# Kernel tuning notes

Measured on AMD Instinct MI355X. Metric: run time of the kernel, lower is better.

## Reference

```python
import jax, jax.numpy as jnp
import numpy as np

N = 100000      # nodes
E = 3200000     # edges
IN, HID, OUT = 512, 256, 16
K = 10
ALPHA = 0.1


def setup_inputs() -> dict:
    key = jax.random.key(0)
    k1, k2, k3, k4 = jax.random.split(key, 4)
    x = jax.random.normal(k1, (N, IN), dtype=jnp.float32)
    edge_index = jax.random.randint(k2, (2, E), 0, N, dtype=jnp.int64)
    # torch.nn.Linear weights are [out_features, in_features]
    W1 = jax.random.normal(k3, (HID, IN), dtype=jnp.float32) * (1.0 / np.sqrt(IN))
    b1 = jnp.zeros((HID,), dtype=jnp.float32)
    W2 = jax.random.normal(k4, (OUT, HID), dtype=jnp.float32) * (1.0 / np.sqrt(HID))
    b2 = jnp.zeros((OUT,), dtype=jnp.float32)
    return {"x": x, "edge_index": edge_index, "W1": W1, "b1": b1, "W2": W2, "b2": b2}


def reference(x, edge_index, W1, b1, W2, b2):
    # Eval mode: dropout(p=0.5) is identity.
    h = jax.nn.relu(x @ W1.T + b1)           # [N, HID]
    h = h @ W2.T + b2                        # [N, OUT]

    # GCN normalization with self loops (PyG gcn_norm, add_self_loops=True)
    loop = jnp.arange(N, dtype=edge_index.dtype)
    row = jnp.concatenate([edge_index[0], loop])   # source (x_j)
    col = jnp.concatenate([edge_index[1], loop])   # target (aggregate here)
    deg = jax.ops.segment_sum(jnp.ones(row.shape[0], dtype=h.dtype), col, num_segments=N)
    dinv = jnp.where(deg > 0, deg ** -0.5, 0.0)
    norm = dinv[row] * dinv[col]                   # [E+N]

    # APPNP: z_{k+1} = (1-alpha) * A_hat z_k + alpha * h
    def step(z, _):
        msg = norm[:, None] * z[row]                                   # [E+N, OUT]
        agg = jax.ops.segment_sum(msg, col, num_segments=N)            # [N, OUT]
        return (1.0 - ALPHA) * agg + ALPHA * h, None

    z, _ = jax.lax.scan(step, h, None, length=K)
    return jax.nn.log_softmax(z, axis=1)
```

## Files before the change

kernel.cpp:

```cpp
#include <hip/hip_runtime.h>
#include <hip/hip_bf16.h>

#define IN_F 512
#define HID_F 256
#define OUT_F 16
#define PHASE_DIV 12512
#define NXCD 8

typedef __bf16 bf8_t __attribute__((ext_vector_type(8)));
typedef float f4_t __attribute__((ext_vector_type(4)));
typedef unsigned short u16x4 __attribute__((ext_vector_type(4)));

__device__ __forceinline__ unsigned short f2b(float f) {
  union { float f; unsigned u; } a; a.f = f;
  unsigned u = a.u;
  u += 0x7fffu + ((u >> 16) & 1u);
  return (unsigned short)(u >> 16);
}

__global__ void detect_k(const int* __restrict__ ei, int* __restrict__ flag) {
  if (threadIdx.x == 0 && blockIdx.x == 0) {
    int is64 = 1;
    for (int i = 0; i < 16; ++i)
      if (ei[2 * i + 1] != 0) is64 = 0;
    *flag = is64;
  }
}

__global__ void cvt_k(const int* __restrict__ ei, int* __restrict__ row32,
                      int* __restrict__ col32, int* __restrict__ cnt,
                      const int* __restrict__ flag, int E_) {
  int e = blockIdx.x * 256 + threadIdx.x;
  if (e >= E_) return;
  int r, c;
  if (*flag) {
    const long long* e64 = (const long long*)ei;
    r = (int)e64[e];
    c = (int)e64[E_ + e];
  } else {
    r = ei[e];
    c = ei[E_ + e];
  }
  row32[e] = r;
  col32[e] = c;
  atomicAdd(&cnt[c], 1);
}

__global__ void dinv_k(const int* __restrict__ cnt, float* __restrict__ dinv, int n) {
  int i = blockIdx.x * 256 + threadIdx.x;
  if (i < n) dinv[i] = rsqrtf((float)(cnt[i] + 1));
}

__global__ __launch_bounds__(256) void mlp_k(
    const float* __restrict__ x, const float* __restrict__ W1,
    const float* __restrict__ b1, const float* __restrict__ W2,
    const float* __restrict__ b2, const float* __restrict__ dinv,
    float* __restrict__ h, float* __restrict__ zs0, int n) {
  __shared__ unsigned short a_sh[64][40];
  __shared__ unsigned short w_sh[256][40];
  __shared__ unsigned short hid_sh[64][264];
  __shared__ unsigned short w2_sh[16][264];
  int tid = threadIdx.x;
  int node0 = blockIdx.x * 64;
  int wvid = tid >> 6;
  int lane = tid & 63;
  int row16 = lane & 15;
  int kg = lane >> 4;

  {
    int r = tid >> 4;
    int c0 = (tid & 15) * 16;
    const float* src = W2 + r * HID_F + c0;
    #pragma unroll
    for (int j = 0; j < 16; j += 4) {
      float4 v = *(const float4*)(src + j);
      u16x4 s = { f2b(v.x), f2b(v.y), f2b(v.z), f2b(v.w) };
      *(u16x4*)&w2_sh[r][c0 + j] = s;
    }
  }

  f4_t acc[4][4];
  #pragma unroll
  for (int mi = 0; mi < 4; ++mi)
    #pragma unroll
    for (int ni = 0; ni < 4; ++ni)
      acc[mi][ni] = (f4_t){0.f, 0.f, 0.f, 0.f};

  for (int kc = 0; kc < 16; ++kc) {
    int kb = kc * 32;
    __syncthreads();
    {
      int r = tid >> 3;
      int c = (tid & 7) * 4;
      #pragma unroll
      for (int p = 0; p < 2; ++p) {
        int rr = p * 32 + r;
        int node = node0 + rr;
        float4 v;
        if (node < n) v = *(const float4*)(x + (size_t)node * IN_F + kb + c);
        else { v.x = 0.f; v.y = 0.f; v.z = 0.f; v.w = 0.f; }
        u16x4 s = { f2b(v.x), f2b(v.y), f2b(v.z), f2b(v.w) };
        *(u16x4*)&a_sh[rr][c] = s;
      }
    }
    {
      int r = tid >> 3;
      int c = (tid & 7) * 4;
      #pragma unroll
      for (int p = 0; p < 8; ++p) {
        int rr = p * 32 + r;
        float4 v = *(const float4*)(W1 + (size_t)rr * IN_F + kb + c);
        u16x4 s = { f2b(v.x), f2b(v.y), f2b(v.z), f2b(v.w) };
        *(u16x4*)&w_sh[rr][c] = s;
      }
    }
    __syncthreads();
    bf8_t af[4], bfr[4];
    #pragma unroll
    for (int mi = 0; mi < 4; ++mi)
      af[mi] = *(const bf8_t*)&a_sh[mi * 16 + row16][kg * 8];
    #pragma unroll
    for (int ni = 0; ni < 4; ++ni)
      bfr[ni] = *(const bf8_t*)&w_sh[wvid * 64 + ni * 16 + row16][kg * 8];
    #pragma unroll
    for (int mi = 0; mi < 4; ++mi)
      #pragma unroll
      for (int ni = 0; ni < 4; ++ni)
        acc[mi][ni] = __builtin_amdgcn_mfma_f32_16x16x32_bf16(af[mi], bfr[ni], acc[mi][ni], 0, 0, 0);
  }
  __syncthreads();
  #pragma unroll
  for (int mi = 0; mi < 4; ++mi) {
    #pragma unroll
    for (int ni = 0; ni < 4; ++ni) {
      int col = wvid * 64 + ni * 16 + row16;
      float bias = b1[col];
      #pragma unroll
      for (int r = 0; r < 4; ++r) {
        int nl = mi * 16 + kg * 4 + r;
        float v = acc[mi][ni][r] + bias;
        v = fmaxf(v, 0.f);
        hid_sh[nl][col] = f2b(v);
      }
    }
  }
  __syncthreads();
  f4_t acc2 = (f4_t){0.f, 0.f, 0.f, 0.f};
  #pragma unroll
  for (int kc = 0; kc < 8; ++kc) {
    bf8_t a2  = *(const bf8_t*)&hid_sh[wvid * 16 + row16][kc * 32 + kg * 8];
    bf8_t b2f = *(const bf8_t*)&w2_sh[row16][kc * 32 + kg * 8];
    acc2 = __builtin_amdgcn_mfma_f32_16x16x32_bf16(a2, b2f, acc2, 0, 0, 0);
  }
  float bias2 = b2[row16];
  #pragma unroll
  for (int r = 0; r < 4; ++r) {
    int nl = wvid * 16 + kg * 4 + r;
    int node = node0 + nl;
    if (node < n) {
      float v = acc2[r] + bias2;
      h[(size_t)node * OUT_F + row16] = v;
      zs0[(size_t)node * OUT_F + row16] = dinv[node] * v;
    }
  }
}

__global__ void scan_blocks(const int* __restrict__ cnt, int* __restrict__ offs,
                            int* __restrict__ bsum, int n) {
  __shared__ int wsum[4];
  int tid = threadIdx.x;
  int base = blockIdx.x * 1024 + tid * 4;
  int v0 = (base + 0 < n) ? cnt[base + 0] : 0;
  int v1 = (base + 1 < n) ? cnt[base + 1] : 0;
  int v2 = (base + 2 < n) ? cnt[base + 2] : 0;
  int v3 = (base + 3 < n) ? cnt[base + 3] : 0;
  int tsum = v0 + v1 + v2 + v3;
  int lane = tid & 63, wv = tid >> 6;
  int inc = tsum;
  #pragma unroll
  for (int off = 1; off < 64; off <<= 1) {
    int t = __shfl_up(inc, off, 64);
    if (lane >= off) inc += t;
  }
  if (lane == 63) wsum[wv] = inc;
  __syncthreads();
  int add = 0;
  #pragma unroll
  for (int j = 0; j < 4; ++j)
    if (j < wv) add += wsum[j];
  int ex = add + inc - tsum;
  if (base + 0 < n) offs[base + 0] = ex;
  if (base + 1 < n) offs[base + 1] = ex + v0;
  if (base + 2 < n) offs[base + 2] = ex + v0 + v1;
  if (base + 3 < n) offs[base + 3] = ex + v0 + v1 + v2;
  if (tid == 255) bsum[blockIdx.x] = add + inc;
}

__global__ void scan_top(int* __restrict__ bsum, int nb) {
  __shared__ int w0;
  int tid = threadIdx.x;
  int v = (tid < nb) ? bsum[tid] : 0;
  int inc = v;
  #pragma unroll
  for (int off = 1; off < 64; off <<= 1) {
    int t = __shfl_up(inc, off, 64);
    if ((tid & 63) >= off) inc += t;
  }
  if (tid == 63) w0 = inc;
  __syncthreads();
  int ex = inc - v + ((tid >= 64) ? w0 : 0);
  if (tid < nb) bsum[tid] = ex;
}

__global__ void scan_add(int* __restrict__ offs, const int* __restrict__ bsum,
                         int* __restrict__ cursor, int n) {
  int base = blockIdx.x * 1024 + threadIdx.x * 4;
  int b = bsum[blockIdx.x];
  #pragma unroll
  for (int j = 0; j < 4; ++j) {
    int i = base + j;
    if (i < n) { int v = offs[i] + b; offs[i] = v; cursor[i] = v; }
  }
}

__global__ __launch_bounds__(256) void scatter_x(
    const int* __restrict__ row32, const int* __restrict__ col32,
    int* __restrict__ cursor, int* __restrict__ nbr, int E_, int nph) {
  int grp = blockIdx.x & (NXCD - 1);
  int bid = blockIdx.x >> 3;
  int nbk = gridDim.x >> 3;
  int stride = nbk * 256;
  for (int p = grp; p < nph; p += NXCD) {
    for (int e = bid * 256 + threadIdx.x; e < E_; e += stride) {
      int c = col32[e];
      if (c / PHASE_DIV == p) {
        int pos = atomicAdd(&cursor[c], 1);
        nbr[pos] = row32[e];
      }
    }
  }
}

__global__ __launch_bounds__(256) void prop_k(
    const float* __restrict__ zs_in, float* __restrict__ zs_out,
    const float* __restrict__ h, const int* __restrict__ offs,
    const int* __restrict__ cnt, const int* __restrict__ nbr,
    const float* __restrict__ dinv, float* __restrict__ out, int fin, int n) {
  int tid = threadIdx.x;
  int node = blockIdx.x * 16 + (tid >> 4);
  int lane = tid & 15;
  if (node >= n) return;
  float di = dinv[node];
  int base = node * OUT_F + lane;
  float a0 = zs_in[base];
  float a1 = 0.f;
  int s = offs[node];
  int end = s + cnt[node];
  int e = s;
  for (; e + 4 <= end; e += 4) {
    int j0 = nbr[e], j1 = nbr[e + 1], j2 = nbr[e + 2], j3 = nbr[e + 3];
    a0 += zs_in[j0 * OUT_F + lane];
    a1 += zs_in[j1 * OUT_F + lane];
    a0 += zs_in[j2 * OUT_F + lane];
    a1 += zs_in[j3 * OUT_F + lane];
  }
  for (; e < end; ++e) a0 += zs_in[nbr[e] * OUT_F + lane];
  float z = 0.9f * di * (a0 + a1) + 0.1f * h[base];
  if (!fin) {
    zs_out[base] = di * z;
  } else {
    float m = z;
    #pragma unroll
    for (int sdx = 8; sdx; sdx >>= 1) m = fmaxf(m, __shfl_xor(m, sdx, 16));
    float ex = expf(z - m);
    float t = ex;
    #pragma unroll
    for (int sdx = 8; sdx; sdx >>= 1) t += __shfl_xor(t, sdx, 16);
    out[base] = z - m - logf(t);
  }
}

extern "C" void kernel_launch(void* const* d_in, const int* in_sizes, int n_in,
                              void* d_out, int out_size, void* d_ws, size_t ws_size,
                              hipStream_t stream) {
  const int Nn = in_sizes[0] / IN_F;
  const int Ee = in_sizes[1] / 2;
  const float* x  = (const float*)d_in[0];
  const int*   ei = (const int*)d_in[1];
  const float* W1 = (const float*)d_in[2];
  const float* b1 = (const float*)d_in[3];
  const float* W2 = (const float*)d_in[4];
  const float* b2 = (const float*)d_in[5];
  float* out = (float*)d_out;

  char* w = (char*)d_ws;
  auto alloc = [&](size_t bytes) {
    char* p = w;
    w += (bytes + 255) & ~(size_t)255;
    return p;
  };
  float* h      = (float*)alloc((size_t)Nn * OUT_F * 4);
  float* zsA    = (float*)alloc((size_t)Nn * OUT_F * 4);
  float* zsB    = (float*)alloc((size_t)Nn * OUT_F * 4);
  int*   cnt    = (int*)alloc((size_t)Nn * 4);
  float* dinv   = (float*)alloc((size_t)Nn * 4);
  int*   offs   = (int*)alloc((size_t)Nn * 4);
  int*   cursor = (int*)alloc((size_t)Nn * 4);
  int*   bsum   = (int*)alloc(1024);
  int*   flag   = (int*)alloc(256);
  int*   nbr    = (int*)alloc((size_t)Ee * 4);
  int*   col32  = (int*)alloc((size_t)Ee * 4);
  int*   row32  = (int*)h;

  hipMemsetAsync(cnt, 0, (size_t)Nn * 4, stream);
  detect_k<<<1, 64, 0, stream>>>(ei, flag);
  cvt_k<<<(Ee + 255) / 256, 256, 0, stream>>>(ei, row32, col32, cnt, flag, Ee);
  dinv_k<<<(Nn + 255) / 256, 256, 0, stream>>>(cnt, dinv, Nn);
  int nb = (Nn + 1023) / 1024;
  scan_blocks<<<nb, 256, 0, stream>>>(cnt, offs, bsum, Nn);
  scan_top<<<1, 128, 0, stream>>>(bsum, nb);
  scan_add<<<nb, 256, 0, stream>>>(offs, bsum, cursor, Nn);
  int nph = (Nn + PHASE_DIV - 1) / PHASE_DIV;
  scatter_x<<<1024, 256, 0, stream>>>(row32, col32, cursor, nbr, Ee, nph);
  mlp_k<<<(Nn + 63) / 64, 256, 0, stream>>>(x, W1, b1, W2, b2, dinv, h, zsA, Nn);

  for (int it = 0; it < 10; ++it) {
    const float* zin = (it & 1) ? zsB : zsA;
    float* zout = (it & 1) ? zsA : zsB;
    int fin = (it == 9) ? 1 : 0;
    prop_k<<<(Nn + 15) / 16, 256, 0, stream>>>(zin, zout, h, offs, cnt, nbr,
                                               dinv, out, fin, Nn);
  }
}
```

Measured before the change: 1.090 ms.

## Pre-convert weights to bf16 once and load W1 fragments directly from global

Adds a small kernel that converts W1 and W2 to bf16 once per call, so each MLP block no longer re-reads and re-converts the full fp32 W1 tile through shared memory. W1 B-fragments are now loaded straight from global/L2 into registers. The K chunk grows from 32 to 64, which halves the number of barrier pairs. The MFMA operands are swapped so each lane holds four consecutive hidden columns, which allows vectorized bias loads and hid_sh stores. In exchange it adds an extra launch and relies on L2 serving the repeated W1 reads from every block.

```diff
diff --git a/kernel.cpp b/kernel.cpp
--- a/kernel.cpp
+++ b/kernel.cpp
@@ -10,6 +10,7 @@
 typedef __bf16 bf8_t __attribute__((ext_vector_type(8)));
 typedef float f4_t __attribute__((ext_vector_type(4)));
 typedef unsigned short u16x4 __attribute__((ext_vector_type(4)));
+typedef unsigned short u16x8 __attribute__((ext_vector_type(8)));
 
 __device__ __forceinline__ unsigned short f2b(float f) {
   union { float f; unsigned u; } a; a.f = f;
@@ -24,6 +25,27 @@
     for (int i = 0; i < 16; ++i)
       if (ei[2 * i + 1] != 0) is64 = 0;
     *flag = is64;
+  }
+}
+
+__global__ void wcvt_k(const float* __restrict__ W1, const float* __restrict__ W2,
+                       unsigned short* __restrict__ W1b, unsigned short* __restrict__ W2b) {
+  int g = blockIdx.x * 256 + threadIdx.x;
+  const int NW1 = (HID_F * IN_F) / 8;
+  const int NW2 = (OUT_F * HID_F) / 8;
+  if (g < NW1) {
+    float4 v0 = ((const float4*)W1)[2 * g];
+    float4 v1 = ((const float4*)W1)[2 * g + 1];
+    u16x8 s = { f2b(v0.x), f2b(v0.y), f2b(v0.z), f2b(v0.w),
+                f2b(v1.x), f2b(v1.y), f2b(v1.z), f2b(v1.w) };
+    ((u16x8*)W1b)[g] = s;
+  } else if (g < NW1 + NW2) {
+    int q = g - NW1;
+    float4 v0 = ((const float4*)W2)[2 * q];
+    float4 v1 = ((const float4*)W2)[2 * q + 1];
+    u16x8 s = { f2b(v0.x), f2b(v0.y), f2b(v0.z), f2b(v0.w),
+                f2b(v1.x), f2b(v1.y), f2b(v1.z), f2b(v1.w) };
+    ((u16x8*)W2b)[q] = s;
   }
 }
 
@@ -52,12 +74,11 @@
 }
 
 __global__ __launch_bounds__(256) void mlp_k(
-    const float* __restrict__ x, const float* __restrict__ W1,
-    const float* __restrict__ b1, const float* __restrict__ W2,
+    const float* __restrict__ x, const unsigned short* __restrict__ W1b,
+    const float* __restrict__ b1, const unsigned short* __restrict__ W2b,
     const float* __restrict__ b2, const float* __restrict__ dinv,
     float* __restrict__ h, float* __restrict__ zs0, int n) {
-  __shared__ unsigned short a_sh[64][40];
-  __shared__ unsigned short w_sh[256][40];
+  __shared__ unsigned short a_sh[64][72];
   __shared__ unsigned short hid_sh[64][264];
   __shared__ unsigned short w2_sh[16][264];
   int tid = threadIdx.x;
@@ -70,13 +91,9 @@
   {
     int r = tid >> 4;
     int c0 = (tid & 15) * 16;
-    const float* src = W2 + r * HID_F + c0;
-    #pragma unroll
-    for (int j = 0; j < 16; j += 4) {
-      float4 v = *(const float4*)(src + j);
-      u16x4 s = { f2b(v.x), f2b(v.y), f2b(v.z), f2b(v.w) };
-      *(u16x4*)&w2_sh[r][c0 + j] = s;
-    }
+    const u16x8* src = (const u16x8*)(W2b + r * HID_F + c0);
+    *(u16x8*)&w2_sh[r][c0] = src[0];
+    *(u16x8*)&w2_sh[r][c0 + 8] = src[1];
   }
 
   f4_t acc[4][4];
@@ -86,62 +103,64 @@
     for (int ni = 0; ni < 4; ++ni)
       acc[mi][ni] = (f4_t){0.f, 0.f, 0.f, 0.f};
 
-  for (int kc = 0; kc < 16; ++kc) {
-    int kb = kc * 32;
+  const unsigned short* wbase = W1b + (size_t)(wvid * 64 + row16) * IN_F + kg * 8;
+
+  int arow = tid >> 2;
+  int acol = (tid & 3) * 16;
+  int anode = node0 + arow;
+  const float* xrow = x + (size_t)anode * IN_F + acol;
+
+  for (int kc = 0; kc < 8; ++kc) {
+    int kb = kc * 64;
     __syncthreads();
     {
-      int r = tid >> 3;
-      int c = (tid & 7) * 4;
-      #pragma unroll
-      for (int p = 0; p < 2; ++p) {
-        int rr = p * 32 + r;
-        int node = node0 + rr;
-        float4 v;
-        if (node < n) v = *(const float4*)(x + (size_t)node * IN_F + kb + c);
-        else { v.x = 0.f; v.y = 0.f; v.z = 0.f; v.w = 0.f; }
-        u16x4 s = { f2b(v.x), f2b(v.y), f2b(v.z), f2b(v.w) };
-        *(u16x4*)&a_sh[rr][c] = s;
+      float4 v0, v1, v2, v3;
+      if (anode < n) {
+        v0 = *(const float4*)(xrow + kb);
+        v1 = *(const float4*)(xrow + kb + 4);
+        v2 = *(const float4*)(xrow + kb + 8);
+        v3 = *(const float4*)(xrow + kb + 12);
+      } else {
+        v0 = v1 = v2 = v3 = (float4){0.f, 0.f, 0.f, 0.f};
       }
-    }
-    {
-      int r = tid >> 3;
-      int c = (tid & 7) * 4;
-      #pragma unroll
-      for (int p = 0; p < 8; ++p) {
-        int rr = p * 32 + r;
-        float4 v = *(const float4*)(W1 + (size_t)rr * IN_F + kb + c);
-        u16x4 s = { f2b(v.x), f2b(v.y), f2b(v.z), f2b(v.w) };
-        *(u16x4*)&w_sh[rr][c] = s;
-      }
+      u16x8 s0 = { f2b(v0.x), f2b(v0.y), f2b(v0.z), f2b(v0.w),
+                   f2b(v1.x), f2b(v1.y), f2b(v1.z), f2b(v1.w) };
+      u16x8 s1 = { f2b(v2.x), f2b(v2.y), f2b(v2.z), f2b(v2.w),
+                   f2b(v3.x), f2b(v3.y), f2b(v3.z), f2b(v3.w) };
+      *(u16x8*)&a_sh[arow][acol] = s0;
+      *(u16x8*)&a_sh[arow][acol + 8] = s1;
     }
     __syncthreads();
-    bf8_t af[4], bfr[4];
-    #pragma unroll
-    for (int mi = 0; mi < 4; ++mi)
-      af[mi] = *(const bf8_t*)&a_sh[mi * 16 + row16][kg * 8];
-    #pragma unroll
-    for (int ni = 0; ni < 4; ++ni)
-      bfr[ni] = *(const bf8_t*)&w_sh[wvid * 64 + ni * 16 + row16][kg * 8];
-    #pragma unroll
-    for (int mi = 0; mi < 4; ++mi)
+    #pragma unroll
+    for (int ks = 0; ks < 2; ++ks) {
+      bf8_t af[4], bfr[4];
       #pragma unroll
       for (int ni = 0; ni < 4; ++ni)
-        acc[mi][ni] = __builtin_amdgcn_mfma_f32_16x16x32_bf16(af[mi], bfr[ni], acc[mi][ni], 0, 0, 0);
+        bfr[ni] = *(const bf8_t*)(wbase + ni * 16 * IN_F + kb + ks * 32);
+      #pragma unroll
+      for (int mi = 0; mi < 4; ++mi)
+        af[mi] = *(const bf8_t*)&a_sh[mi * 16 + row16][ks * 32 + kg * 8];
+      #pragma unroll
+      for (int mi = 0; mi < 4; ++mi)
+        #pragma unroll
+        for (int ni = 0; ni < 4; ++ni)
+          acc[mi][ni] = __builtin_amdgcn_mfma_f32_16x16x32_bf16(bfr[ni], af[mi], acc[mi][ni], 0, 0, 0);
+    }
   }
   __syncthreads();
   #pragma unroll
-  for (int mi = 0; mi < 4; ++mi) {
-    #pragma unroll
-    for (int ni = 0; ni < 4; ++ni) {
-      int col = wvid * 64 + ni * 16 + row16;
-      float bias = b1[col];
-      #pragma unroll
-      for (int r = 0; r < 4; ++r) {
-        int nl = mi * 16 + kg * 4 + r;
-        float v = acc[mi][ni][r] + bias;
-        v = fmaxf(v, 0.f);
-        hid_sh[nl][col] = f2b(v);
-      }
+  for (int ni = 0; ni < 4; ++ni) {
+    int hb = wvid * 64 + ni * 16 + kg * 4;
+    float4 bias4 = *(const float4*)&b1[hb];
+    #pragma unroll
+    for (int mi = 0; mi < 4; ++mi) {
+      int nl = mi * 16 + row16;
+      float v0 = fmaxf(acc[mi][ni][0] + bias4.x, 0.f);
+      float v1 = fmaxf(acc[mi][ni][1] + bias4.y, 0.f);
+      float v2 = fmaxf(acc[mi][ni][2] + bias4.z, 0.f);
+      float v3 = fmaxf(acc[mi][ni][3] + bias4.w, 0.f);
+      u16x4 s = { f2b(v0), f2b(v1), f2b(v2), f2b(v3) };
+      *(u16x4*)&hid_sh[nl][hb] = s;
     }
   }
   __syncthreads();
@@ -310,10 +329,13 @@
   int*   flag   = (int*)alloc(256);
   int*   nbr    = (int*)alloc((size_t)Ee * 4);
   int*   col32  = (int*)alloc((size_t)Ee * 4);
+  unsigned short* W1b = (unsigned short*)alloc((size_t)HID_F * IN_F * 2);
+  unsigned short* W2b = (unsigned short*)alloc((size_t)OUT_F * HID_F * 2);
   int*   row32  = (int*)h;
 
   hipMemsetAsync(cnt, 0, (size_t)Nn * 4, stream);
   detect_k<<<1, 64, 0, stream>>>(ei, flag);
+  wcvt_k<<<66, 256, 0, stream>>>(W1, W2, W1b, W2b);
   cvt_k<<<(Ee + 255) / 256, 256, 0, stream>>>(ei, row32, col32, cnt, flag, Ee);
   dinv_k<<<(Nn + 255) / 256, 256, 0, stream>>>(cnt, dinv, Nn);
   int nb = (Nn + 1023) / 1024;
@@ -322,7 +344,7 @@
   scan_add<<<nb, 256, 0, stream>>>(offs, bsum, cursor, Nn);
   int nph = (Nn + PHASE_DIV - 1) / PHASE_DIV;
   scatter_x<<<1024, 256, 0, stream>>>(row32, col32, cursor, nbr, Ee, nph);
-  mlp_k<<<(Nn + 63) / 64, 256, 0, stream>>>(x, W1, b1, W2, b2, dinv, h, zsA, Nn);
+  mlp_k<<<(Nn + 63) / 64, 256, 0, stream>>>(x, W1b, b1, W2b, b2, dinv, h, zsA, Nn);
 
   for (int it = 0; it < 10; ++it) {
     const float* zin = (it & 1) ? zsB : zsA;
```

After: 1.035 ms. 5.0% less time.
